# Kernel tuning notes

Hardware: AMD Instinct MI355X
Metric: run time of the kernel (lower is better)

## Reference

```python
import jax, jax.numpy as jnp
import numpy as np

EPS = 1e-3  # keras LayerNormalization default epsilon

def layer_norm(x, gamma, beta):
    mu = jnp.mean(x, axis=-1, keepdims=True)
    var = jnp.var(x, axis=-1, keepdims=True)
    return (x - mu) * jax.lax.rsqrt(var + EPS) * gamma + beta

def setup_inputs() -> dict:
    key = jax.random.key(0)
    ks = jax.random.split(key, 10)
    B, N, FD, AD, PD, DP = 4, 512, 256, 256, 128, 64
    s = lambda k, *sh: jax.random.normal(k, sh, dtype=jnp.float32)
    return {
        "F": s(ks[0], B, N, FD),
        "D": s(ks[1], B, N, N, DP),
        "Wq": s(ks[2], FD, AD) / np.sqrt(FD),
        "Wk": s(ks[3], FD, AD) / np.sqrt(FD),
        "Wv": s(ks[4], FD, AD) / np.sqrt(FD),
        "g_f": jnp.ones((FD,), jnp.float32),
        "b_f": jnp.zeros((FD,), jnp.float32),
        "g_p": jnp.ones((DP,), jnp.float32),
        "b_p": jnp.zeros((DP,), jnp.float32),
        "W_pt": s(ks[5], DP, PD) / np.sqrt(DP),
        "b_pt": jnp.zeros((PD,), jnp.float32),
        "W_ph": s(ks[6], PD, 1) / np.sqrt(PD),
    }

def reference(F, D, Wq, Wk, Wv, g_f, b_f, g_p, b_p, W_pt, b_pt, W_ph):
    # features path
    Fn = layer_norm(F, g_f, b_f)                       # [B,N,FD]
    Q = Fn @ Wq                                        # [B,N,AD]
    K = Fn @ Wk
    V = Fn @ Wv
    # pair-bias path: LN -> Dense(pairs_dim)+bias -> Dense(num_heads=1)
    Bn = layer_norm(D, g_p, b_p)                       # [B,N,N,DP]
    Bt = Bn @ W_pt + b_pt                              # [B,N,N,PD]
    bias = (Bt @ W_ph)[..., 0]                         # [B,N,N]
    scalar = 1.0 / jnp.sqrt(jnp.float32(Q.shape[-1]))
    A = jnp.einsum('bqd,bkd->bqk', Q, K) + bias        # QK^T + pair bias
    A = jax.nn.softmax(scalar * A, axis=-1)
    O = jnp.einsum('bqk,bkd->bqd', A, V)               # [B,N,AD]
    return jnp.sum(O, axis=-1)                         # [B,N]
```

## Files before the change

### kernel.cpp

```cpp
#include <hip/hip_runtime.h>
#include <hip/hip_bf16.h>
#include <cstddef>

#define OFF_GW    0
#define OFF_WV    64
#define OFF_SC    320
#define OFF_VSUM  384
#define OFF_Q     2432
#define OFF_K     526720
#define OFF_SB    1051008

__global__ __launch_bounds__(256) void k0_consts(
    const float* __restrict__ Wv, const float* __restrict__ g_p,
    const float* __restrict__ b_p, const float* __restrict__ W_pt,
    const float* __restrict__ b_pt, const float* __restrict__ W_ph,
    float* __restrict__ ws) {
  int t = threadIdx.x;
  if (blockIdx.x < 64) {
    int row = blockIdx.x * 4 + (t >> 6);
    int l = t & 63;
    float s = 0.f;
#pragma unroll
    for (int j = 0; j < 4; ++j) s += Wv[row * 256 + l + 64 * j];
    for (int m = 32; m >= 1; m >>= 1) s += __shfl_xor(s, m);
    if (l == 0) ws[OFF_WV + row] = s;
  } else {
    __shared__ float wc_s[64];
    __shared__ float wph_s[128];
    if (t < 128) wph_s[t] = W_ph[t];
    __syncthreads();
    int c = t >> 2, sub = t & 3;
    float wc = 0.f;
#pragma unroll
    for (int j = 0; j < 32; ++j)
      wc += W_pt[c * 128 + sub * 32 + j] * wph_s[sub * 32 + j];
    wc += __shfl_xor(wc, 1);
    wc += __shfl_xor(wc, 2);
    if (sub == 0) {
      wc_s[c] = wc;
      ws[OFF_GW + c] = g_p[c] * wc;
    }
    __syncthreads();
    if (t == 0) {
      float sg = 0.f, bc = 0.f;
      for (int cc = 0; cc < 64; ++cc) {
        sg += g_p[cc] * wc_s[cc];
        bc += b_p[cc] * wc_s[cc];
      }
      for (int p = 0; p < 128; ++p) bc += b_pt[p] * wph_s[p];
      ws[OFF_SC] = sg;
      ws[OFF_SC + 1] = bc;
    }
  }
}

__global__ __launch_bounds__(256) void k1_ln_qk(
    const float* __restrict__ F, const float* __restrict__ Wq,
    const float* __restrict__ Wk, const float* __restrict__ g_f,
    const float* __restrict__ b_f, float* __restrict__ ws) {
  __shared__ float fn[8][257];
  __shared__ float smu[8], srn[8];
  int t = threadIdx.x;
  int row0 = blockIdx.x * 8;
  const float* Fp = F + (size_t)row0 * 256;
#pragma unroll
  for (int k = 0; k < 8; ++k) fn[k][t] = Fp[k * 256 + t];
  __syncthreads();
  int r = t >> 5, l32 = t & 31;
  float s1 = 0.f, s2 = 0.f;
#pragma unroll
  for (int m = 0; m < 8; ++m) {
    float x = fn[r][l32 + 32 * m];
    s1 += x;
    s2 += x * x;
  }
  for (int m = 16; m >= 1; m >>= 1) {
    s1 += __shfl_xor(s1, m);
    s2 += __shfl_xor(s2, m);
  }
  if (l32 == 0) {
    float mu = s1 * (1.f / 256.f);
    float var = s2 * (1.f / 256.f) - mu * mu;
    smu[r] = mu;
    srn[r] = rsqrtf(var + 1e-3f);
  }
  __syncthreads();
  float gf = g_f[t], bf = b_f[t];
#pragma unroll
  for (int k = 0; k < 8; ++k)
    fn[k][t] = (fn[k][t] - smu[k]) * srn[k] * gf + bf;
  __syncthreads();
  {
    const float* wv = ws + OFF_WV;
    float s = 0.f;
#pragma unroll
    for (int m = 0; m < 8; ++m) s += fn[r][l32 + 32 * m] * wv[l32 + 32 * m];
    for (int m = 16; m >= 1; m >>= 1) s += __shfl_xor(s, m);
    if (l32 == 0) ws[OFF_VSUM + row0 + r] = s;
  }
  float qa[8] = {0, 0, 0, 0, 0, 0, 0, 0};
  float ka[8] = {0, 0, 0, 0, 0, 0, 0, 0};
  for (int f = 0; f < 256; ++f) {
    float wq = Wq[f * 256 + t];
    float wk = Wk[f * 256 + t];
#pragma unroll
    for (int k = 0; k < 8; ++k) {
      float x = fn[k][f];
      qa[k] += x * wq;
      ka[k] += x * wk;
    }
  }
  float* Qo = ws + OFF_Q + (size_t)row0 * 256;
  float* Ko = ws + OFF_K + (size_t)row0 * 256;
#pragma unroll
  for (int k = 0; k < 8; ++k) {
    Qo[k * 256 + t] = qa[k];
    Ko[k * 256 + t] = ka[k];
  }
}

__global__ __launch_bounds__(256) void k2_bias(const float* __restrict__ D,
                                               float* __restrict__ ws) {
  int tid = blockIdx.x * 256 + threadIdx.x;
  int e = tid >> 2;
  int q = tid & 3;
  const float4* dp = (const float4*)(D + (size_t)e * 64 + q * 16);
  const float4* gw4 = (const float4*)(ws + OFF_GW) + q * 4;
  float s1 = 0.f, s2 = 0.f, sw = 0.f;
#pragma unroll
  for (int j = 0; j < 4; ++j) {
    float4 x = dp[j];
    float4 g = gw4[j];
    s1 += x.x + x.y + x.z + x.w;
    s2 += x.x * x.x + x.y * x.y + x.z * x.z + x.w * x.w;
    sw += x.x * g.x + x.y * g.y + x.z * g.z + x.w * g.w;
  }
  s1 += __shfl_xor(s1, 1);
  s2 += __shfl_xor(s2, 1);
  sw += __shfl_xor(sw, 1);
  s1 += __shfl_xor(s1, 2);
  s2 += __shfl_xor(s2, 2);
  sw += __shfl_xor(sw, 2);
  if (q == 0) {
    float mu = s1 * (1.f / 64.f);
    float var = s2 * (1.f / 64.f) - mu * mu;
    float rn = rsqrtf(var + 1e-3f);
    float sum_gw = ws[OFF_SC];
    float bconst = ws[OFF_SC + 1];
    ws[OFF_SB + e] = (rn * (sw - mu * sum_gw) + bconst) * 0.0625f;
  }
}

__global__ __launch_bounds__(256) void k3_attn(const float* __restrict__ ws,
                                               float* __restrict__ out) {
  __shared__ float4 Qs4[4][64];
  __shared__ float Sx[4][512];
  __shared__ float vs[512];
  int t = threadIdx.x;
  int b = blockIdx.x >> 7;
  int tile = blockIdx.x & 127;
  int q0 = tile * 4;
  int rowbase = b * 512 + q0;
  const float* Qg = ws + OFF_Q;
  const float* Kg = ws + OFF_K;
  float* qsf = (float*)Qs4;
#pragma unroll
  for (int k = 0; k < 4; ++k) qsf[k * 256 + t] = Qg[(size_t)(rowbase + k) * 256 + t];
  vs[t] = ws[OFF_VSUM + b * 512 + t];
  vs[t + 256] = ws[OFF_VSUM + b * 512 + 256 + t];
  __syncthreads();
  const float4* K0p = (const float4*)(Kg + (size_t)(b * 512 + t) * 256);
  const float4* K1p = (const float4*)(Kg + (size_t)(b * 512 + 256 + t) * 256);
  float a0[4] = {0, 0, 0, 0}, a1[4] = {0, 0, 0, 0};
  for (int f = 0; f < 64; ++f) {
    float4 kv0 = K0p[f];
    float4 kv1 = K1p[f];
#pragma unroll
    for (int rr = 0; rr < 4; ++rr) {
      float4 qv = Qs4[rr][f];
      a0[rr] += qv.x * kv0.x + qv.y * kv0.y + qv.z * kv0.z + qv.w * kv0.w;
      a1[rr] += qv.x * kv1.x + qv.y * kv1.y + qv.z * kv1.z + qv.w * kv1.w;
    }
  }
  const float* sb = ws + OFF_SB;
#pragma unroll
  for (int rr = 0; rr < 4; ++rr) {
    size_t sbrow = (size_t)(rowbase + rr) * 512;
    Sx[rr][t] = a0[rr] * 0.0625f + sb[sbrow + t];
    Sx[rr][t + 256] = a1[rr] * 0.0625f + sb[sbrow + 256 + t];
  }
  __syncthreads();
  int w = t >> 6, l = t & 63;
  float m = -1e30f;
#pragma unroll
  for (int j = 0; j < 8; ++j) m = fmaxf(m, Sx[w][l + 64 * j]);
  for (int mm = 32; mm >= 1; mm >>= 1) m = fmaxf(m, __shfl_xor(m, mm));
  float se = 0.f, sv = 0.f;
#pragma unroll
  for (int j = 0; j < 8; ++j) {
    float ev = __expf(Sx[w][l + 64 * j] - m);
    se += ev;
    sv += ev * vs[l + 64 * j];
  }
  for (int mm = 32; mm >= 1; mm >>= 1) {
    se += __shfl_xor(se, mm);
    sv += __shfl_xor(sv, mm);
  }
  if (l == 0) out[rowbase + w] = sv / se;
}

extern "C" void kernel_launch(void* const* d_in, const int* in_sizes, int n_in,
                              void* d_out, int out_size, void* d_ws,
                              size_t ws_size, hipStream_t stream) {
  const float* F    = (const float*)d_in[0];
  const float* D    = (const float*)d_in[1];
  const float* Wq   = (const float*)d_in[2];
  const float* Wk   = (const float*)d_in[3];
  const float* Wv   = (const float*)d_in[4];
  const float* g_f  = (const float*)d_in[5];
  const float* b_f  = (const float*)d_in[6];
  const float* g_p  = (const float*)d_in[7];
  const float* b_p  = (const float*)d_in[8];
  const float* W_pt = (const float*)d_in[9];
  const float* b_pt = (const float*)d_in[10];
  const float* W_ph = (const float*)d_in[11];
  float* out = (float*)d_out;
  float* ws = (float*)d_ws;

  k0_consts<<<65, 256, 0, stream>>>(Wv, g_p, b_p, W_pt, b_pt, W_ph, ws);
  k1_ln_qk<<<256, 256, 0, stream>>>(F, Wq, Wk, g_f, b_f, ws);
  k2_bias<<<16384, 256, 0, stream>>>(D, ws);
  k3_attn<<<512, 256, 0, stream>>>(ws, out);
}
```

Baseline: 457.9 us.

## Fuse pair-bias LayerNorm into attention kernel and split QK projection blocks

```diff
diff --git a/kernel.cpp b/kernel.cpp
--- a/kernel.cpp
+++ b/kernel.cpp
@@ -8,7 +8,6 @@
 #define OFF_VSUM  384
 #define OFF_Q     2432
 #define OFF_K     526720
-#define OFF_SB    1051008
 
 __global__ __launch_bounds__(256) void k0_consts(
     const float* __restrict__ Wv, const float* __restrict__ g_p,
@@ -61,7 +60,8 @@
   __shared__ float fn[8][257];
   __shared__ float smu[8], srn[8];
   int t = threadIdx.x;
-  int row0 = blockIdx.x * 8;
+  int g = blockIdx.x >> 1, h = blockIdx.x & 1;
+  int row0 = g * 8;
   const float* Fp = F + (size_t)row0 * 256;
 #pragma unroll
   for (int k = 0; k < 8; ++k) fn[k][t] = Fp[k * 256 + t];
@@ -90,7 +90,7 @@
   for (int k = 0; k < 8; ++k)
     fn[k][t] = (fn[k][t] - smu[k]) * srn[k] * gf + bf;
   __syncthreads();
-  {
+  if (h == 0) {
     const float* wv = ws + OFF_WV;
     float s = 0.f;
 #pragma unroll
@@ -98,61 +98,24 @@
     for (int m = 16; m >= 1; m >>= 1) s += __shfl_xor(s, m);
     if (l32 == 0) ws[OFF_VSUM + row0 + r] = s;
   }
-  float qa[8] = {0, 0, 0, 0, 0, 0, 0, 0};
-  float ka[8] = {0, 0, 0, 0, 0, 0, 0, 0};
+  int matsel = t >> 7;
+  int col = h * 128 + (t & 127);
+  const float* W = matsel ? Wk : Wq;
+  float acc[8] = {0, 0, 0, 0, 0, 0, 0, 0};
+#pragma unroll 4
   for (int f = 0; f < 256; ++f) {
-    float wq = Wq[f * 256 + t];
-    float wk = Wk[f * 256 + t];
-#pragma unroll
-    for (int k = 0; k < 8; ++k) {
-      float x = fn[k][f];
-      qa[k] += x * wq;
-      ka[k] += x * wk;
-    }
-  }
-  float* Qo = ws + OFF_Q + (size_t)row0 * 256;
-  float* Ko = ws + OFF_K + (size_t)row0 * 256;
-#pragma unroll
-  for (int k = 0; k < 8; ++k) {
-    Qo[k * 256 + t] = qa[k];
-    Ko[k * 256 + t] = ka[k];
-  }
-}
-
-__global__ __launch_bounds__(256) void k2_bias(const float* __restrict__ D,
-                                               float* __restrict__ ws) {
-  int tid = blockIdx.x * 256 + threadIdx.x;
-  int e = tid >> 2;
-  int q = tid & 3;
-  const float4* dp = (const float4*)(D + (size_t)e * 64 + q * 16);
-  const float4* gw4 = (const float4*)(ws + OFF_GW) + q * 4;
-  float s1 = 0.f, s2 = 0.f, sw = 0.f;
-#pragma unroll
-  for (int j = 0; j < 4; ++j) {
-    float4 x = dp[j];
-    float4 g = gw4[j];
-    s1 += x.x + x.y + x.z + x.w;
-    s2 += x.x * x.x + x.y * x.y + x.z * x.z + x.w * x.w;
-    sw += x.x * g.x + x.y * g.y + x.z * g.z + x.w * g.w;
-  }
-  s1 += __shfl_xor(s1, 1);
-  s2 += __shfl_xor(s2, 1);
-  sw += __shfl_xor(sw, 1);
-  s1 += __shfl_xor(s1, 2);
-  s2 += __shfl_xor(s2, 2);
-  sw += __shfl_xor(sw, 2);
-  if (q == 0) {
-    float mu = s1 * (1.f / 64.f);
-    float var = s2 * (1.f / 64.f) - mu * mu;
-    float rn = rsqrtf(var + 1e-3f);
-    float sum_gw = ws[OFF_SC];
-    float bconst = ws[OFF_SC + 1];
-    ws[OFF_SB + e] = (rn * (sw - mu * sum_gw) + bconst) * 0.0625f;
-  }
-}
-
-__global__ __launch_bounds__(256) void k3_attn(const float* __restrict__ ws,
-                                               float* __restrict__ out) {
+    float w = W[f * 256 + col];
+#pragma unroll
+    for (int k = 0; k < 8; ++k) acc[k] += fn[k][f] * w;
+  }
+  float* Out = ws + (matsel ? OFF_K : OFF_Q) + (size_t)row0 * 256 + col;
+#pragma unroll
+  for (int k = 0; k < 8; ++k) Out[k * 256] = acc[k];
+}
+
+__global__ __launch_bounds__(256) void kb_bias_attn(
+    const float* __restrict__ D, const float* __restrict__ ws,
+    float* __restrict__ out) {
   __shared__ float4 Qs4[4][64];
   __shared__ float Sx[4][512];
   __shared__ float vs[512];
@@ -161,17 +124,55 @@
   int tile = blockIdx.x & 127;
   int q0 = tile * 4;
   int rowbase = b * 512 + q0;
-  const float* Qg = ws + OFF_Q;
-  const float* Kg = ws + OFF_K;
   float* qsf = (float*)Qs4;
 #pragma unroll
-  for (int k = 0; k < 4; ++k) qsf[k * 256 + t] = Qg[(size_t)(rowbase + k) * 256 + t];
+  for (int k = 0; k < 4; ++k)
+    qsf[k * 256 + t] = ws[OFF_Q + (size_t)(rowbase + k) * 256 + t];
   vs[t] = ws[OFF_VSUM + b * 512 + t];
   vs[t + 256] = ws[OFF_VSUM + b * 512 + 256 + t];
-  __syncthreads();
+  float sum_gw = ws[OFF_SC];
+  float bconst = ws[OFF_SC + 1];
+  int qq = t & 3;
+  float4 g[4];
+#pragma unroll
+  for (int j = 0; j < 4; ++j) g[j] = ((const float4*)(ws + OFF_GW))[qq * 4 + j];
+
+  int e4 = t >> 2;
+  const float* Dbase = D + (size_t)rowbase * 512 * 64;
+#pragma unroll 4
+  for (int pi = 0; pi < 32; ++pi) {
+    int rr = pi >> 3;
+    int kk = (pi & 7) * 64 + e4;
+    const float4* dp =
+        (const float4*)(Dbase + ((size_t)rr * 512 + kk) * 64 + qq * 16);
+    float s1 = 0.f, s2 = 0.f, sw = 0.f;
+#pragma unroll
+    for (int j = 0; j < 4; ++j) {
+      float4 x = dp[j];
+      s1 += x.x + x.y + x.z + x.w;
+      s2 += x.x * x.x + x.y * x.y + x.z * x.z + x.w * x.w;
+      sw += x.x * g[j].x + x.y * g[j].y + x.z * g[j].z + x.w * g[j].w;
+    }
+    s1 += __shfl_xor(s1, 1);
+    s2 += __shfl_xor(s2, 1);
+    sw += __shfl_xor(sw, 1);
+    s1 += __shfl_xor(s1, 2);
+    s2 += __shfl_xor(s2, 2);
+    sw += __shfl_xor(sw, 2);
+    if (qq == 0) {
+      float mu = s1 * (1.f / 64.f);
+      float var = s2 * (1.f / 64.f) - mu * mu;
+      float rn = rsqrtf(var + 1e-3f);
+      Sx[rr][kk] = (rn * (sw - mu * sum_gw) + bconst) * 0.0625f;
+    }
+  }
+  __syncthreads();
+
+  const float* Kg = ws + OFF_K;
   const float4* K0p = (const float4*)(Kg + (size_t)(b * 512 + t) * 256);
   const float4* K1p = (const float4*)(Kg + (size_t)(b * 512 + 256 + t) * 256);
   float a0[4] = {0, 0, 0, 0}, a1[4] = {0, 0, 0, 0};
+#pragma unroll 4
   for (int f = 0; f < 64; ++f) {
     float4 kv0 = K0p[f];
     float4 kv1 = K1p[f];
@@ -182,14 +183,13 @@
       a1[rr] += qv.x * kv1.x + qv.y * kv1.y + qv.z * kv1.z + qv.w * kv1.w;
     }
   }
-  const float* sb = ws + OFF_SB;
 #pragma unroll
   for (int rr = 0; rr < 4; ++rr) {
-    size_t sbrow = (size_t)(rowbase + rr) * 512;
-    Sx[rr][t] = a0[rr] * 0.0625f + sb[sbrow + t];
-    Sx[rr][t + 256] = a1[rr] * 0.0625f + sb[sbrow + 256 + t];
-  }
-  __syncthreads();
+    Sx[rr][t] += a0[rr] * 0.0625f;
+    Sx[rr][t + 256] += a1[rr] * 0.0625f;
+  }
+  __syncthreads();
+
   int w = t >> 6, l = t & 63;
   float m = -1e30f;
 #pragma unroll
@@ -228,7 +228,6 @@
   float* ws = (float*)d_ws;
 
   k0_consts<<<65, 256, 0, stream>>>(Wv, g_p, b_p, W_pt, b_pt, W_ph, ws);
-  k1_ln_qk<<<256, 256, 0, stream>>>(F, Wq, Wk, g_f, b_f, ws);
-  k2_bias<<<16384, 256, 0, stream>>>(D, ws);
-  k3_attn<<<512, 256, 0, stream>>>(ws, out);
-}
+  k1_ln_qk<<<512, 256, 0, stream>>>(F, Wq, Wk, g_f, b_f, ws);
+  kb_bias_attn<<<512, 256, 0, stream>>>(D, ws, out);
+}
```

Measured after the change: 450.9 us. About the same (-1.5%).
